# Kernel tuning notes

Hardware: AMD Instinct MI355X
Metric: run time of the kernel (lower is better)

## Reference

```python
import jax, jax.numpy as jnp
import numpy as np

TOP_K = 2
CAPACITY_FACTOR = 1.25
LOAD_BALANCE_WEIGHT = 0.01
ROUTER_Z_WEIGHT = 0.001


def setup_inputs() -> dict:
    key = jax.random.key(0)
    k1, k2, k3, k4, k5 = jax.random.split(key, 5)
    B, S, D, F, E = 4, 2048, 1024, 4096, 8
    x = jax.random.normal(k1, (B, S, D), dtype=jnp.float32)
    gate_w = jax.random.normal(k2, (E, D), dtype=jnp.float32) * 0.02
    wi_gate = jax.random.normal(k3, (E, F, D), dtype=jnp.float32) * 0.02
    wi_up = jax.random.normal(k4, (E, F, D), dtype=jnp.float32) * 0.02
    wo = jax.random.normal(k5, (E, D, F), dtype=jnp.float32) * 0.02
    return {"x": x, "gate_w": gate_w, "wi_gate": wi_gate, "wi_up": wi_up, "wo": wo}


def _dispatch_combine_one_k(x_flat, eids, ew, wi_gate, wi_up, wo, capacity):
    """Capacity-limited dispatch (first-come positions), GeGLU expert, combine."""
    N, D = x_flat.shape
    E = wi_gate.shape[0]
    # position of each token within its expert's queue (count of earlier tokens
    # assigned to the same expert) -- matches the atomic counter semantics in order.
    oh = jax.nn.one_hot(eids, E, dtype=jnp.int32)            # [N, E]
    pos = jnp.cumsum(oh, axis=0) - oh                        # counts strictly before
    pos = jnp.take_along_axis(pos, eids[:, None], axis=1)[:, 0]  # [N]
    valid = pos < capacity
    pos_safe = jnp.where(valid, pos, capacity)               # overflow bucket
    # dispatched_x[e, c, :] = x of the token at slot (e, c); zeros where empty
    disp = jnp.zeros((E, capacity + 1, D), x_flat.dtype).at[eids, pos_safe].set(x_flat)
    disp = disp[:, :capacity]                                # drop overflow bucket
    # grouped GeGLU expert: batched GEMMs over experts
    gate_h = jax.nn.silu(jnp.einsum('ecd,efd->ecf', disp, wi_gate))
    up_h = jnp.einsum('ecd,efd->ecf', disp, wi_up)
    eout = jnp.einsum('ecf,edf->ecd', gate_h * up_h, wo)     # [E, cap, D]
    # combine: gather each token's expert output, weight, zero dropped tokens
    y = eout[eids, jnp.minimum(pos, capacity - 1)]           # [N, D]
    return y * (ew * valid.astype(x_flat.dtype))[:, None]


def reference(x, gate_w, wi_gate, wi_up, wo):
    B, S, D = x.shape
    E = gate_w.shape[0]
    N = B * S
    capacity = max(int(N / E * CAPACITY_FACTOR), 1)
    x_flat = x.reshape(N, D)
    router_logits = x_flat @ gate_w.T                        # [N, E]
    router_probs = jax.nn.softmax(router_logits, axis=-1)
    topk_probs, topk_idx = jax.lax.top_k(router_probs, TOP_K)
    topk_probs = topk_probs / jnp.sum(topk_probs, axis=-1, keepdims=True)
    out = jnp.zeros_like(x_flat)
    for k in range(TOP_K):
        out = out + _dispatch_combine_one_k(
            x_flat, topk_idx[:, k], topk_probs[:, k], wi_gate, wi_up, wo, capacity)
    # aux losses: Switch-style load balance + router z-loss
    density = jnp.mean(jax.nn.one_hot(topk_idx, E, dtype=x.dtype).sum(axis=1), axis=0) / TOP_K
    mean_probs = jnp.mean(router_probs, axis=0)
    lb_loss = LOAD_BALANCE_WEIGHT * E * jnp.sum(density * mean_probs)
    z_loss = ROUTER_Z_WEIGHT * jnp.mean(jax.scipy.special.logsumexp(router_logits, axis=-1) ** 2)
    aux_loss = lb_loss + z_loss
    return out.reshape(B, S, D), aux_loss
```

## Files before the change

kernel.cpp:

```cpp
#include <hip/hip_runtime.h>
#include <cstdint>
#include <cstddef>

#define N_TOK 8192
#define DDIM  1024
#define FDIM  4096
#define NEXP  8
#define CAP   1280
#define MPE   2560
#define NSLOT (NEXP * MPE)

typedef __attribute__((ext_vector_type(8))) __bf16 bf16x8;
typedef __attribute__((ext_vector_type(4))) float  f32x4;

__device__ __forceinline__ unsigned short f2bf(float f) {
    unsigned int u = __float_as_uint(f);
    u += 0x7fffu + ((u >> 16) & 1u);
    return (unsigned short)(u >> 16);
}
__device__ __forceinline__ float bf2f(unsigned short s) {
    return __uint_as_float(((unsigned int)s) << 16);
}

__device__ __forceinline__ void async_cp16(const void* g, void* l) {
    __builtin_amdgcn_global_load_lds(
        (const __attribute__((address_space(1))) unsigned int*)g,
        (__attribute__((address_space(3))) unsigned int*)l, 16, 0, 0);
}

__global__ __launch_bounds__(256) void convert_wi_kernel(
    const float* __restrict__ wi_gate, const float* __restrict__ wi_up,
    unsigned short* __restrict__ wcomb)
{
    const int idx = blockIdx.x * 256 + threadIdx.x;
    const int d8 = idx & 127;
    const int r  = (idx >> 7) & 8191;
    const int e  = idx >> 20;
    const int f  = (r >> 7) * 64 + (r & 63);
    const float* src = (((r >> 6) & 1) ? wi_up : wi_gate)
                       + ((size_t)(e * FDIM + f) * DDIM + d8 * 8);
    const float4 a = ((const float4*)src)[0];
    const float4 b = ((const float4*)src)[1];
    uint4 o;
    o.x = (unsigned)f2bf(a.x) | ((unsigned)f2bf(a.y) << 16);
    o.y = (unsigned)f2bf(a.z) | ((unsigned)f2bf(a.w) << 16);
    o.z = (unsigned)f2bf(b.x) | ((unsigned)f2bf(b.y) << 16);
    o.w = (unsigned)f2bf(b.z) | ((unsigned)f2bf(b.w) << 16);
    *(uint4*)(wcomb + (size_t)idx * 8) = o;
}

__global__ __launch_bounds__(256) void convert_wo_kernel(
    const float* __restrict__ wo, unsigned short* __restrict__ wo_bf)
{
    const int idx = blockIdx.x * 256 + threadIdx.x;
    const float4 a = ((const float4*)(wo + (size_t)idx * 8))[0];
    const float4 b = ((const float4*)(wo + (size_t)idx * 8))[1];
    uint4 o;
    o.x = (unsigned)f2bf(a.x) | ((unsigned)f2bf(a.y) << 16);
    o.y = (unsigned)f2bf(a.z) | ((unsigned)f2bf(a.w) << 16);
    o.z = (unsigned)f2bf(b.x) | ((unsigned)f2bf(b.y) << 16);
    o.w = (unsigned)f2bf(b.z) | ((unsigned)f2bf(b.w) << 16);
    *(uint4*)(wo_bf + (size_t)idx * 8) = o;
}

__global__ __launch_bounds__(256) void router_kernel(
    const float* __restrict__ x, const float* __restrict__ gate_w,
    int* __restrict__ topk_idx, float* __restrict__ topk_w,
    float* __restrict__ stats)
{
    const int wave = threadIdx.x >> 6, lane = threadIdx.x & 63;
    const int n = blockIdx.x * 4 + wave;
    const float4* xp = (const float4*)(x + (size_t)n * DDIM + lane * 16);
    float4 xv[4];
#pragma unroll
    for (int i = 0; i < 4; i++) xv[i] = xp[i];
    float part[NEXP];
#pragma unroll
    for (int e = 0; e < NEXP; e++) {
        const float4* gp = (const float4*)(gate_w + (size_t)e * DDIM + lane * 16);
        float s = 0.f;
#pragma unroll
        for (int i = 0; i < 4; i++) {
            const float4 g = gp[i];
            s += xv[i].x * g.x + xv[i].y * g.y + xv[i].z * g.z + xv[i].w * g.w;
        }
        part[e] = s;
    }
#pragma unroll
    for (int off = 32; off > 0; off >>= 1)
#pragma unroll
        for (int e = 0; e < NEXP; e++) part[e] += __shfl_down(part[e], off);
    if (lane == 0) {
        float p[NEXP];
        float m = -1e30f;
#pragma unroll
        for (int e = 0; e < NEXP; e++) m = fmaxf(m, part[e]);
        float sum = 0.f;
#pragma unroll
        for (int e = 0; e < NEXP; e++) { p[e] = __expf(part[e] - m); sum += p[e]; }
        const float inv = 1.f / sum;
#pragma unroll
        for (int e = 0; e < NEXP; e++) p[e] *= inv;
        const float lse = m + __logf(sum);
        int e1 = 0; float p1 = p[0];
#pragma unroll
        for (int e = 1; e < NEXP; e++) if (p[e] > p1) { p1 = p[e]; e1 = e; }
        int e2 = -1; float p2 = -1.f;
#pragma unroll
        for (int e = 0; e < NEXP; e++) if (e != e1 && p[e] > p2) { p2 = p[e]; e2 = e; }
        const float wsum = p1 + p2;
        topk_idx[n * 2 + 0] = e1; topk_idx[n * 2 + 1] = e2;
        topk_w[n * 2 + 0] = p1 / wsum; topk_w[n * 2 + 1] = p2 / wsum;
        float* sp = stats + (n & 63) * 17;
#pragma unroll
        for (int e = 0; e < NEXP; e++) atomicAdd(sp + e, p[e]);
        atomicAdd(sp + 8 + e1, 1.f);
        atomicAdd(sp + 8 + e2, 1.f);
        atomicAdd(sp + 16, lse * lse);
    }
}

__global__ __launch_bounds__(512) void pos_kernel(
    const int* __restrict__ topk_idx, const float* __restrict__ topk_w,
    int* __restrict__ slot_tok, int* __restrict__ tok2slot, int* __restrict__ gcnt)
{
    __shared__ int cnt[2][NEXP][256];
    const int t = threadIdx.x;
    for (int i = t; i < NSLOT; i += 512) slot_tok[i] = -1;
    const int kk = t >> 8;
    const int c  = t & 255;
    int lc[NEXP];
#pragma unroll
    for (int e = 0; e < NEXP; e++) lc[e] = 0;
    const int base_n = c * 32;
    for (int i = 0; i < 32; i++) lc[topk_idx[(base_n + i) * 2 + kk]]++;
#pragma unroll
    for (int e = 0; e < NEXP; e++) cnt[kk][e][c] = lc[e];
    __syncthreads();
    if (t < 16) {
        const int k2 = t >> 3, e = t & 7;
        int run = 0;
        for (int c2 = 0; c2 < 256; c2++) { int v = cnt[k2][e][c2]; cnt[k2][e][c2] = run; run += v; }
        gcnt[e * 2 + k2] = run < CAP ? run : CAP;
    }
    __syncthreads();
    int run[NEXP];
#pragma unroll
    for (int e = 0; e < NEXP; e++) run[e] = cnt[kk][e][c];
    for (int i = 0; i < 32; i++) {
        const int n = base_n + i;
        const int e = topk_idx[n * 2 + kk];
        const int p = run[e]++;
        if (p < CAP) {
            const int slot = (e * 2 + kk) * CAP + p;
            slot_tok[slot] = n;
            tok2slot[n * 2 + kk] = slot;
        } else {
            tok2slot[n * 2 + kk] = -1;
        }
    }
}

__global__ __launch_bounds__(128) void dispatch_kernel(
    const float* __restrict__ x, const int* __restrict__ slot_tok,
    unsigned short* __restrict__ disp)
{
    const int slot = blockIdx.x;
    const int t = threadIdx.x;
    const int token = slot_tok[slot];
    uint4 o = make_uint4(0u, 0u, 0u, 0u);
    if (token >= 0) {
        const float4* src = (const float4*)(x + (size_t)token * DDIM + t * 8);
        const float4 a = src[0];
        const float4 b = src[1];
        o.x = (unsigned)f2bf(a.x) | ((unsigned)f2bf(a.y) << 16);
        o.y = (unsigned)f2bf(a.z) | ((unsigned)f2bf(a.w) << 16);
        o.z = (unsigned)f2bf(b.x) | ((unsigned)f2bf(b.y) << 16);
        o.w = (unsigned)f2bf(b.z) | ((unsigned)f2bf(b.w) << 16);
    }
    *(uint4*)(disp + (size_t)slot * DDIM + t * 8) = o;
}

__global__ __launch_bounds__(256, 3) void gemm1_kernel(
    const unsigned short* __restrict__ disp,
    const unsigned short* __restrict__ wcomb,
    const int* __restrict__ gcnt,
    unsigned short* __restrict__ act)
{
    __shared__ __align__(16) unsigned short smem[8704];
    const int b = blockIdx.x;
    const int e   = b / 1280;
    const int rem = b % 1280;
    const int mb = rem / 64, nb = rem % 64;
    const int kk = mb / 10;
    if ((mb % 10) * 128 >= gcnt[e * 2 + kk]) return;

    const int t = threadIdx.x;
    const int wave = t >> 6, lane = t & 63;
    const unsigned short* Asrc = disp  + (size_t)(e * MPE + mb * 128) * DDIM;
    const unsigned short* Bsrc = wcomb + (size_t)e * 8192 * DDIM + (size_t)(nb * 128) * DDIM;

    const int arow = t >> 2;
    const int acol = (((t & 3) ^ ((arow >> 1) & 3)) * 8);

    const f32x4 fzero = {0.f, 0.f, 0.f, 0.f};
    f32x4 acc[4][4];
#pragma unroll
    for (int i = 0; i < 4; i++)
#pragma unroll
        for (int j = 0; j < 4; j++) acc[i][j] = fzero;

    const int wm = wave >> 1, wn = wave & 1;
    const int lrow = lane & 15, lk = lane >> 4;
    const int lkx = (lk ^ ((lrow >> 1) & 3)) * 8;

    for (int k0 = 0; k0 < DDIM; k0 += 32) {
        __syncthreads();
        async_cp16(Asrc + (size_t)arow * DDIM + k0 + acol,        &smem[wave * 512]);
        async_cp16(Asrc + (size_t)(arow + 64) * DDIM + k0 + acol, &smem[2048 + wave * 512]);
        async_cp16(Bsrc + (size_t)arow * DDIM + k0 + acol,        &smem[4096 + wave * 512]);
        async_cp16(Bsrc + (size_t)(arow + 64) * DDIM + k0 + acol, &smem[6144 + wave * 512]);
        __syncthreads();
        bf16x8 af[4], bfr[4];
#pragma unroll
        for (int i = 0; i < 4; i++)
            af[i] = *(const bf16x8*)&smem[(wm * 64 + i * 16 + lrow) * 32 + lkx];
#pragma unroll
        for (int j = 0; j < 4; j++)
            bfr[j] = *(const bf16x8*)&smem[4096 + (wn * 64 + j * 16 + lrow) * 32 + lkx];
#pragma unroll
        for (int i = 0; i < 4; i++)
#pragma unroll
            for (int j = 0; j < 4; j++)
                acc[i][j] = __builtin_amdgcn_mfma_f32_16x16x32_bf16(af[i], bfr[j], acc[i][j], 0, 0, 0);
    }

    __syncthreads();
    if (wn == 0) {
#pragma unroll
        for (int i = 0; i < 4; i++)
#pragma unroll
            for (int j = 0; j < 4; j++)
#pragma unroll
                for (int r = 0; r < 4; r++)
                    smem[(wm * 64 + i * 16 + lk * 4 + r) * 68 + j * 16 + lrow] = f2bf(acc[i][j][r]);
    }
    __syncthreads();
    if (wn == 1) {
#pragma unroll
        for (int i = 0; i < 4; i++)
#pragma unroll
            for (int r = 0; r < 4; r++) {
                const int m = wm * 64 + i * 16 + lk * 4 + r;
                const size_t base = (size_t)(e * MPE + mb * 128 + m) * FDIM + nb * 64;
#pragma unroll
                for (int j = 0; j < 4; j++) {
                    const float g = bf2f(smem[m * 68 + j * 16 + lrow]);
                    const float u = acc[i][j][r];
                    const float a = (g / (1.f + __expf(-g))) * u;
                    act[base + j * 16 + lrow] = f2bf(a);
                }
            }
    }
}

__global__ __launch_bounds__(256, 3) void gemm2_kernel(
    const unsigned short* __restrict__ act,
    const unsigned short* __restrict__ wo_bf,
    const int* __restrict__ gcnt,
    unsigned short* __restrict__ eout)
{
    __shared__ __align__(16) unsigned short smem[8192];
    const int b = blockIdx.x;
    const int e   = b / 160;
    const int rem = b % 160;
    const int mb = rem / 8, nb = rem % 8;
    const int kk = mb / 10;
    if ((mb % 10) * 128 >= gcnt[e * 2 + kk]) return;

    const int t = threadIdx.x;
    const int wave = t >> 6, lane = t & 63;
    const unsigned short* Asrc = act   + (size_t)(e * MPE + mb * 128) * FDIM;
    const unsigned short* Bsrc = wo_bf + (size_t)e * DDIM * FDIM + (size_t)(nb * 128) * FDIM;

    const int arow = t >> 2;
    const int acol = (((t & 3) ^ ((arow >> 1) & 3)) * 8);

    const f32x4 fzero = {0.f, 0.f, 0.f, 0.f};
    f32x4 acc[4][4];
#pragma unroll
    for (int i = 0; i < 4; i++)
#pragma unroll
        for (int j = 0; j < 4; j++) acc[i][j] = fzero;

    const int wm = wave >> 1, wn = wave & 1;
    const int lrow = lane & 15, lk = lane >> 4;
    const int lkx = (lk ^ ((lrow >> 1) & 3)) * 8;

    for (int k0 = 0; k0 < FDIM; k0 += 32) {
        __syncthreads();
        async_cp16(Asrc + (size_t)arow * FDIM + k0 + acol,        &smem[wave * 512]);
        async_cp16(Asrc + (size_t)(arow + 64) * FDIM + k0 + acol, &smem[2048 + wave * 512]);
        async_cp16(Bsrc + (size_t)arow * FDIM + k0 + acol,        &smem[4096 + wave * 512]);
        async_cp16(Bsrc + (size_t)(arow + 64) * FDIM + k0 + acol, &smem[6144 + wave * 512]);
        __syncthreads();
        bf16x8 af[4], bfr[4];
#pragma unroll
        for (int i = 0; i < 4; i++)
            af[i] = *(const bf16x8*)&smem[(wm * 64 + i * 16 + lrow) * 32 + lkx];
#pragma unroll
        for (int j = 0; j < 4; j++)
            bfr[j] = *(const bf16x8*)&smem[4096 + (wn * 64 + j * 16 + lrow) * 32 + lkx];
#pragma unroll
        for (int i = 0; i < 4; i++)
#pragma unroll
            for (int j = 0; j < 4; j++)
                acc[i][j] = __builtin_amdgcn_mfma_f32_16x16x32_bf16(af[i], bfr[j], acc[i][j], 0, 0, 0);
    }
#pragma unroll
    for (int i = 0; i < 4; i++)
#pragma unroll
        for (int r = 0; r < 4; r++) {
            const int srow = e * MPE + mb * 128 + wm * 64 + i * 16 + lk * 4 + r;
            const size_t obase = (size_t)srow * DDIM + nb * 128 + wn * 64;
#pragma unroll
            for (int j = 0; j < 4; j++)
                eout[obase + j * 16 + lrow] = f2bf(acc[i][j][r]);
        }
}

__global__ __launch_bounds__(256) void combine_kernel(
    const unsigned short* __restrict__ eout,
    const int* __restrict__ tok2slot, const float* __restrict__ topk_w,
    float* __restrict__ out)
{
    const int n = blockIdx.x;
    const int t = threadIdx.x;
    const int s0 = tok2slot[n * 2 + 0], s1 = tok2slot[n * 2 + 1];
    const float w0 = (s0 >= 0) ? topk_w[n * 2 + 0] : 0.f;
    const float w1 = (s1 >= 0) ? topk_w[n * 2 + 1] : 0.f;
    const int a0 = (s0 >= 0) ? s0 : 0;
    const int a1 = (s1 >= 0) ? s1 : 0;
    const uint2 p0 = *(const uint2*)(eout + (size_t)a0 * DDIM + t * 4);
    const uint2 p1 = *(const uint2*)(eout + (size_t)a1 * DDIM + t * 4);
    float4 o;
    o.x = w0 * bf2f((unsigned short)(p0.x & 0xffff)) + w1 * bf2f((unsigned short)(p1.x & 0xffff));
    o.y = w0 * bf2f((unsigned short)(p0.x >> 16))    + w1 * bf2f((unsigned short)(p1.x >> 16));
    o.z = w0 * bf2f((unsigned short)(p0.y & 0xffff)) + w1 * bf2f((unsigned short)(p1.y & 0xffff));
    o.w = w0 * bf2f((unsigned short)(p0.y >> 16))    + w1 * bf2f((unsigned short)(p1.y >> 16));
    *(float4*)(out + (size_t)n * DDIM + t * 4) = o;
}

__global__ void aux_kernel(const float* __restrict__ stats, float* __restrict__ out)
{
    if (threadIdx.x == 0 && blockIdx.x == 0) {
        float ps[NEXP], cn[NEXP], z = 0.f;
#pragma unroll
        for (int e = 0; e < NEXP; e++) { ps[e] = 0.f; cn[e] = 0.f; }
        for (int c = 0; c < 64; c++) {
            const float* sp = stats + c * 17;
#pragma unroll
            for (int e = 0; e < NEXP; e++) { ps[e] += sp[e]; cn[e] += sp[8 + e]; }
            z += sp[16];
        }
        float lb = 0.f;
#pragma unroll
        for (int e = 0; e < NEXP; e++)
            lb += (cn[e] / (2.f * N_TOK)) * (ps[e] / N_TOK);
        const float aux = 0.01f * 8.f * lb + 0.001f * (z / N_TOK);
        out[(size_t)N_TOK * DDIM] = aux;
    }
}

extern "C" void kernel_launch(void* const* d_in, const int* in_sizes, int n_in,
                              void* d_out, int out_size, void* d_ws, size_t ws_size,
                              hipStream_t stream)
{
    (void)in_sizes; (void)n_in; (void)ws_size; (void)out_size;
    const float* x       = (const float*)d_in[0];
    const float* gate_w  = (const float*)d_in[1];
    const float* wi_gate = (const float*)d_in[2];
    const float* wi_up   = (const float*)d_in[3];
    const float* wo      = (const float*)d_in[4];
    float* out = (float*)d_out;
    char* ws = (char*)d_ws;

    int*            topk_idx = (int*)(ws + 0);
    float*          topk_w   = (float*)(ws + 65536);
    int*            slot_tok = (int*)(ws + 131072);
    int*            tok2slot = (int*)(ws + 212992);
    float*          stats    = (float*)(ws + 278528);
    int*            gcnt     = (int*)(ws + 282880);
    unsigned short* disp     = (unsigned short*)(ws + 524288);
    unsigned short* act      = (unsigned short*)(ws + 42467328);
    unsigned short* eout     = (unsigned short*)(ws + 210239488);
    unsigned short* wcomb    = (unsigned short*)(ws + 252182528);
    unsigned short* wo_bf    = (unsigned short*)(ws + 386400256);

    hipMemsetAsync(stats, 0, 64 * 17 * sizeof(float), stream);

    convert_wi_kernel<<<32768, 256, 0, stream>>>(wi_gate, wi_up, wcomb);
    convert_wo_kernel<<<16384, 256, 0, stream>>>(wo, wo_bf);
    router_kernel<<<N_TOK / 4, 256, 0, stream>>>(x, gate_w, topk_idx, topk_w, stats);
    pos_kernel<<<1, 512, 0, stream>>>(topk_idx, topk_w, slot_tok, tok2slot, gcnt);
    dispatch_kernel<<<NSLOT, 128, 0, stream>>>(x, slot_tok, disp);
    gemm1_kernel<<<NEXP * 20 * 64, 256, 0, stream>>>(disp, wcomb, gcnt, act);
    gemm2_kernel<<<NEXP * 20 * 8, 256, 0, stream>>>(act, wo_bf, gcnt, eout);
    combine_kernel<<<N_TOK, 256, 0, stream>>>(eout, tok2slot, topk_w, out);
    aux_kernel<<<1, 64, 0, stream>>>(stats, out);
}
```

Measured before the change: 1.116 ms.

## Enlarge gemm1 tiles to 256x256 with triple-buffered async LDS pipeline

Rewrites the first expert GEMM so each 512-thread block computes a 256x256 tile instead of 128x128. K-tiles are staged into LDS through a three-deep ring of async copies, with split A/B prefetches interleaved between MFMA halves and s_setprio raised around the compute. The aim is to raise arithmetic intensity and hide global load latency behind MFMA work. In exchange, LDS and register use grow (96KB LDS, 128 accumulator floats per thread), which cuts occupancy, and capacity skipping becomes coarser at 256-row granularity.

```diff
diff --git a/kernel.cpp b/kernel.cpp
--- a/kernel.cpp
+++ b/kernel.cpp
@@ -181,83 +181,124 @@
     *(uint4*)(disp + (size_t)slot * DDIM + t * 8) = o;
 }
 
-__global__ __launch_bounds__(256, 3) void gemm1_kernel(
+__global__ __launch_bounds__(512, 2) void gemm1_kernel(
     const unsigned short* __restrict__ disp,
     const unsigned short* __restrict__ wcomb,
     const int* __restrict__ gcnt,
     unsigned short* __restrict__ act)
 {
-    __shared__ __align__(16) unsigned short smem[8704];
+    __shared__ __align__(16) unsigned short smem[49152];
     const int b = blockIdx.x;
-    const int e   = b / 1280;
-    const int rem = b % 1280;
-    const int mb = rem / 64, nb = rem % 64;
-    const int kk = mb / 10;
-    if ((mb % 10) * 128 >= gcnt[e * 2 + kk]) return;
+    const int e    = b / 320;
+    const int rem  = b % 320;
+    const int kk   = rem / 160;
+    const int rem2 = rem % 160;
+    const int mt = rem2 / 32, nt = rem2 % 32;
+    if (mt * 256 >= gcnt[e * 2 + kk]) return;
 
     const int t = threadIdx.x;
     const int wave = t >> 6, lane = t & 63;
-    const unsigned short* Asrc = disp  + (size_t)(e * MPE + mb * 128) * DDIM;
-    const unsigned short* Bsrc = wcomb + (size_t)e * 8192 * DDIM + (size_t)(nb * 128) * DDIM;
-
-    const int arow = t >> 2;
-    const int acol = (((t & 3) ^ ((arow >> 1) & 3)) * 8);
-
-    const f32x4 fzero = {0.f, 0.f, 0.f, 0.f};
-    f32x4 acc[4][4];
-#pragma unroll
-    for (int i = 0; i < 4; i++)
-#pragma unroll
-        for (int j = 0; j < 4; j++) acc[i][j] = fzero;
-
-    const int wm = wave >> 1, wn = wave & 1;
+    const unsigned short* Asrc = disp  + (size_t)(e * MPE + kk * CAP + mt * 256) * DDIM;
+    const unsigned short* Bsrc = wcomb + (size_t)e * 8192 * DDIM + (size_t)(nt * 256) * DDIM;
+
+    const int srow = t >> 2;
+    const int qg   = (((t & 3) ^ ((srow >> 1) & 3)) * 8);
+    const size_t soff0 = (size_t)srow * DDIM + qg;
+    const size_t soff1 = (size_t)(srow + 128) * DDIM + qg;
+    const int lb0 = wave * 512;
+    const int lb1 = 4096 + wave * 512;
+
+#define G1_STAGE_A(c, kt) do { \
+        async_cp16(Asrc + soff0 + (size_t)(kt) * 32, &smem[(c) * 16384 + lb0]); \
+        async_cp16(Asrc + soff1 + (size_t)(kt) * 32, &smem[(c) * 16384 + lb1]); } while (0)
+#define G1_STAGE_B(c, kt) do { \
+        async_cp16(Bsrc + soff0 + (size_t)(kt) * 32, &smem[(c) * 16384 + 8192 + lb0]); \
+        async_cp16(Bsrc + soff1 + (size_t)(kt) * 32, &smem[(c) * 16384 + 8192 + lb1]); } while (0)
+
+    const int wm = wave >> 2, wn = wave & 3;
     const int lrow = lane & 15, lk = lane >> 4;
     const int lkx = (lk ^ ((lrow >> 1) & 3)) * 8;
-
-    for (int k0 = 0; k0 < DDIM; k0 += 32) {
-        __syncthreads();
-        async_cp16(Asrc + (size_t)arow * DDIM + k0 + acol,        &smem[wave * 512]);
-        async_cp16(Asrc + (size_t)(arow + 64) * DDIM + k0 + acol, &smem[2048 + wave * 512]);
-        async_cp16(Bsrc + (size_t)arow * DDIM + k0 + acol,        &smem[4096 + wave * 512]);
-        async_cp16(Bsrc + (size_t)(arow + 64) * DDIM + k0 + acol, &smem[6144 + wave * 512]);
-        __syncthreads();
+    const int aro = (wm * 128 + lrow) * 32 + lkx;
+    const int bro = 8192 + (wn * 64 + lrow) * 32 + lkx;
+
+    const f32x4 fzero = {0.f, 0.f, 0.f, 0.f};
+    f32x4 acc[8][4];
+#pragma unroll
+    for (int i = 0; i < 8; i++)
+#pragma unroll
+        for (int j = 0; j < 4; j++) acc[i][j] = fzero;
+
+    G1_STAGE_A(0, 0); G1_STAGE_B(0, 0);
+    G1_STAGE_A(1, 1); G1_STAGE_B(1, 1);
+    asm volatile("s_waitcnt vmcnt(4)" ::: "memory");
+    __builtin_amdgcn_s_barrier();
+
+    int cur = 0;
+#pragma unroll 1
+    for (int kt = 0; kt < 32; ++kt) {
+        const int cbase = cur * 16384;
+        int cnxt = cur + 2; if (cnxt >= 3) cnxt -= 3;
+        const bool pf = (kt + 2 < 32);
         bf16x8 af[4], bfr[4];
 #pragma unroll
-        for (int i = 0; i < 4; i++)
-            af[i] = *(const bf16x8*)&smem[(wm * 64 + i * 16 + lrow) * 32 + lkx];
-#pragma unroll
-        for (int j = 0; j < 4; j++)
-            bfr[j] = *(const bf16x8*)&smem[4096 + (wn * 64 + j * 16 + lrow) * 32 + lkx];
+        for (int i = 0; i < 4; i++) af[i]  = *(const bf16x8*)&smem[cbase + aro + i * 512];
+#pragma unroll
+        for (int j = 0; j < 4; j++) bfr[j] = *(const bf16x8*)&smem[cbase + bro + j * 512];
+        if (pf) G1_STAGE_A(cnxt, kt + 2);
+        __builtin_amdgcn_s_barrier();
+        __builtin_amdgcn_s_setprio(1);
 #pragma unroll
         for (int i = 0; i < 4; i++)
 #pragma unroll
             for (int j = 0; j < 4; j++)
                 acc[i][j] = __builtin_amdgcn_mfma_f32_16x16x32_bf16(af[i], bfr[j], acc[i][j], 0, 0, 0);
-    }
+        __builtin_amdgcn_s_setprio(0);
+        __builtin_amdgcn_s_barrier();
+        bf16x8 ag[4];
+#pragma unroll
+        for (int i = 0; i < 4; i++) ag[i] = *(const bf16x8*)&smem[cbase + aro + (i + 4) * 512];
+        if (pf) G1_STAGE_B(cnxt, kt + 2);
+        __builtin_amdgcn_s_barrier();
+        __builtin_amdgcn_s_setprio(1);
+#pragma unroll
+        for (int i = 0; i < 4; i++)
+#pragma unroll
+            for (int j = 0; j < 4; j++)
+                acc[i + 4][j] = __builtin_amdgcn_mfma_f32_16x16x32_bf16(ag[i], bfr[j], acc[i + 4][j], 0, 0, 0);
+        __builtin_amdgcn_s_setprio(0);
+        if (pf) asm volatile("s_waitcnt vmcnt(4)" ::: "memory");
+        else    asm volatile("s_waitcnt vmcnt(0)" ::: "memory");
+        __builtin_amdgcn_s_barrier();
+        cur = cur + 1; if (cur == 3) cur = 0;
+    }
+#undef G1_STAGE_A
+#undef G1_STAGE_B
 
     __syncthreads();
-    if (wn == 0) {
-#pragma unroll
-        for (int i = 0; i < 4; i++)
+    const int g = wn >> 1;
+    const int epb = g * 17408;
+    if ((wn & 1) == 0) {
+#pragma unroll
+        for (int i = 0; i < 8; i++)
 #pragma unroll
             for (int j = 0; j < 4; j++)
 #pragma unroll
                 for (int r = 0; r < 4; r++)
-                    smem[(wm * 64 + i * 16 + lk * 4 + r) * 68 + j * 16 + lrow] = f2bf(acc[i][j][r]);
+                    smem[epb + (wm * 128 + i * 16 + lk * 4 + r) * 68 + j * 16 + lrow] = f2bf(acc[i][j][r]);
     }
     __syncthreads();
-    if (wn == 1) {
-#pragma unroll
-        for (int i = 0; i < 4; i++)
+    if (wn & 1) {
+#pragma unroll
+        for (int i = 0; i < 8; i++)
 #pragma unroll
             for (int r = 0; r < 4; r++) {
-                const int m = wm * 64 + i * 16 + lk * 4 + r;
-                const size_t base = (size_t)(e * MPE + mb * 128 + m) * FDIM + nb * 64;
+                const int m = wm * 128 + i * 16 + lk * 4 + r;
+                const size_t base = (size_t)(e * MPE + kk * CAP + mt * 256 + m) * FDIM + (nt * 2 + g) * 64;
 #pragma unroll
                 for (int j = 0; j < 4; j++) {
-                    const float g = bf2f(smem[m * 68 + j * 16 + lrow]);
-                    const float u = acc[i][j][r];
-                    const float a = (g / (1.f + __expf(-g))) * u;
+                    const float gv = bf2f(smem[epb + m * 68 + j * 16 + lrow]);
+                    const float u  = acc[i][j][r];
+                    const float a  = (gv / (1.f + __expf(-gv))) * u;
                     act[base + j * 16 + lrow] = f2bf(a);
                 }
             }
@@ -404,7 +445,7 @@
     router_kernel<<<N_TOK / 4, 256, 0, stream>>>(x, gate_w, topk_idx, topk_w, stats);
     pos_kernel<<<1, 512, 0, stream>>>(topk_idx, topk_w, slot_tok, tok2slot, gcnt);
     dispatch_kernel<<<NSLOT, 128, 0, stream>>>(x, slot_tok, disp);
-    gemm1_kernel<<<NEXP * 20 * 64, 256, 0, stream>>>(disp, wcomb, gcnt, act);
+    gemm1_kernel<<<NEXP * 2 * 5 * 32, 512, 0, stream>>>(disp, wcomb, gcnt, act);
     gemm2_kernel<<<NEXP * 20 * 8, 256, 0, stream>>>(act, wo_bf, gcnt, eout);
     combine_kernel<<<N_TOK, 256, 0, stream>>>(eout, tok2slot, topk_w, out);
     aux_kernel<<<1, 64, 0, stream>>>(stats, out);
```

New measurement: 1.147 ms. +2.8%, slower.

## Replace expert GEMMs with 256x256-tile, 4-stage pipelined 512-thread template kernel

Applied to the files above, without the earlier changes.

Both expert GEMMs (gate/up with GeGLU epilogue, and down projection) are replaced by one templated kernel. It uses 256x256 output tiles, 8 waves per block and a 4-deep LDS ring of async copies with explicit vmcnt waits, plus register double-buffered fragment reads. This is meant to raise data reuse per tile and overlap global loads with MFMA, instead of the old synchronous single-stage 128x128 loop. In exchange it uses 128KB of shared memory per block, which limits occupancy. The larger tiles also mean fewer blocks, coarser capacity skipping and more padded rows.

```diff
diff --git a/kernel.cpp b/kernel.cpp
--- a/kernel.cpp
+++ b/kernel.cpp
@@ -181,152 +181,135 @@
     *(uint4*)(disp + (size_t)slot * DDIM + t * 8) = o;
 }
 
-__global__ __launch_bounds__(256, 3) void gemm1_kernel(
-    const unsigned short* __restrict__ disp,
-    const unsigned short* __restrict__ wcomb,
+template<int KDIM, int BROWS, int NT, int EPI>
+__global__ __launch_bounds__(512, 2) void gemm256(
+    const unsigned short* __restrict__ A,
+    const unsigned short* __restrict__ Bw,
     const int* __restrict__ gcnt,
-    unsigned short* __restrict__ act)
-{
-    __shared__ __align__(16) unsigned short smem[8704];
+    unsigned short* __restrict__ outp)
+{
+    constexpr int NKT = KDIM / 32;
+    __shared__ __align__(16) unsigned short smem[65536];
     const int b = blockIdx.x;
-    const int e   = b / 1280;
-    const int rem = b % 1280;
-    const int mb = rem / 64, nb = rem % 64;
-    const int kk = mb / 10;
-    if ((mb % 10) * 128 >= gcnt[e * 2 + kk]) return;
+    const int e    = b / (2 * 5 * NT);
+    const int rem  = b % (2 * 5 * NT);
+    const int kk   = rem / (5 * NT);
+    const int rem2 = rem % (5 * NT);
+    const int mt = rem2 / NT, nt = rem2 % NT;
+    if (mt * 256 >= gcnt[e * 2 + kk]) return;
 
     const int t = threadIdx.x;
     const int wave = t >> 6, lane = t & 63;
-    const unsigned short* Asrc = disp  + (size_t)(e * MPE + mb * 128) * DDIM;
-    const unsigned short* Bsrc = wcomb + (size_t)e * 8192 * DDIM + (size_t)(nb * 128) * DDIM;
-
-    const int arow = t >> 2;
-    const int acol = (((t & 3) ^ ((arow >> 1) & 3)) * 8);
-
-    const f32x4 fzero = {0.f, 0.f, 0.f, 0.f};
-    f32x4 acc[4][4];
-#pragma unroll
-    for (int i = 0; i < 4; i++)
-#pragma unroll
-        for (int j = 0; j < 4; j++) acc[i][j] = fzero;
-
-    const int wm = wave >> 1, wn = wave & 1;
+    const unsigned short* Asrc = A  + (size_t)(e * MPE + kk * CAP + mt * 256) * KDIM;
+    const unsigned short* Bsrc = Bw + ((size_t)e * BROWS + (size_t)nt * 256) * KDIM;
+
+    const int srow = t >> 2;
+    const int qg   = (((t & 3) ^ ((srow >> 1) & 3)) * 8);
+    const size_t soff0 = (size_t)srow * KDIM + qg;
+    const size_t soff1 = (size_t)(srow + 128) * KDIM + qg;
+    const int lb0 = wave * 512, lb1 = 4096 + wave * 512;
+
+#define STG(c, kt) do { \
+        const size_t ko_ = (size_t)(kt) * 32; \
+        async_cp16(Asrc + soff0 + ko_, &smem[(c) * 16384 + lb0]); \
+        async_cp16(Asrc + soff1 + ko_, &smem[(c) * 16384 + lb1]); \
+        async_cp16(Bsrc + soff0 + ko_, &smem[(c) * 16384 + 8192 + lb0]); \
+        async_cp16(Bsrc + soff1 + ko_, &smem[(c) * 16384 + 8192 + lb1]); } while (0)
+
+    const int wm = wave >> 2, wn = wave & 3;
     const int lrow = lane & 15, lk = lane >> 4;
     const int lkx = (lk ^ ((lrow >> 1) & 3)) * 8;
-
-    for (int k0 = 0; k0 < DDIM; k0 += 32) {
+    const int aro = (wm * 128 + lrow) * 32 + lkx;
+    const int bro = 8192 + (wn * 64 + lrow) * 32 + lkx;
+
+    const f32x4 fzero = {0.f, 0.f, 0.f, 0.f};
+    f32x4 acc[8][4];
+#pragma unroll
+    for (int i = 0; i < 8; i++)
+#pragma unroll
+        for (int j = 0; j < 4; j++) acc[i][j] = fzero;
+
+#define RD(SA, SB, c) do { \
+        _Pragma("unroll") for (int i_ = 0; i_ < 8; i_++) \
+            SA[i_] = *(const bf16x8*)&smem[(c) * 16384 + aro + i_ * 512]; \
+        _Pragma("unroll") for (int j_ = 0; j_ < 4; j_++) \
+            SB[j_] = *(const bf16x8*)&smem[(c) * 16384 + bro + j_ * 512]; } while (0)
+
+#define MM(SA, SB) do { \
+        __builtin_amdgcn_s_setprio(1); \
+        _Pragma("unroll") for (int i_ = 0; i_ < 8; i_++) \
+            _Pragma("unroll") for (int j_ = 0; j_ < 4; j_++) \
+                acc[i_][j_] = __builtin_amdgcn_mfma_f32_16x16x32_bf16(SA[i_], SB[j_], acc[i_][j_], 0, 0, 0); \
+        __builtin_amdgcn_s_setprio(0); } while (0)
+
+#define BODY(kt, CA, CB, NA, NB) do { \
+        if ((kt) < NKT - 2) asm volatile("s_waitcnt vmcnt(4)" ::: "memory"); \
+        else                asm volatile("s_waitcnt vmcnt(0)" ::: "memory"); \
+        __builtin_amdgcn_s_barrier(); \
+        if ((kt) + 1 < NKT) RD(NA, NB, ((kt) + 1) & 3); \
+        if ((kt) + 3 < NKT) STG(((kt) + 3) & 3, (kt) + 3); \
+        __builtin_amdgcn_sched_barrier(0); \
+        MM(CA, CB); } while (0)
+
+    STG(0, 0); STG(1, 1); STG(2, 2);
+    asm volatile("s_waitcnt vmcnt(8)" ::: "memory");
+    __builtin_amdgcn_s_barrier();
+
+    bf16x8 afA[8], bfA[4], afB[8], bfB[4];
+    RD(afA, bfA, 0);
+
+#pragma unroll 1
+    for (int m = 0; m < NKT / 2; m++) {
+        BODY(2 * m,     afA, bfA, afB, bfB);
+        BODY(2 * m + 1, afB, bfB, afA, bfA);
+    }
+#undef BODY
+#undef MM
+#undef RD
+#undef STG
+
+    if constexpr (EPI == 1) {
         __syncthreads();
-        async_cp16(Asrc + (size_t)arow * DDIM + k0 + acol,        &smem[wave * 512]);
-        async_cp16(Asrc + (size_t)(arow + 64) * DDIM + k0 + acol, &smem[2048 + wave * 512]);
-        async_cp16(Bsrc + (size_t)arow * DDIM + k0 + acol,        &smem[4096 + wave * 512]);
-        async_cp16(Bsrc + (size_t)(arow + 64) * DDIM + k0 + acol, &smem[6144 + wave * 512]);
+        const int g = wn >> 1;
+        const int epb = g * 17408;
+        if ((wn & 1) == 0) {
+#pragma unroll
+            for (int i = 0; i < 8; i++)
+#pragma unroll
+                for (int j = 0; j < 4; j++)
+#pragma unroll
+                    for (int r = 0; r < 4; r++)
+                        smem[epb + (wm * 128 + i * 16 + lk * 4 + r) * 68 + j * 16 + lrow] = f2bf(acc[i][j][r]);
+        }
         __syncthreads();
-        bf16x8 af[4], bfr[4];
-#pragma unroll
-        for (int i = 0; i < 4; i++)
-            af[i] = *(const bf16x8*)&smem[(wm * 64 + i * 16 + lrow) * 32 + lkx];
-#pragma unroll
-        for (int j = 0; j < 4; j++)
-            bfr[j] = *(const bf16x8*)&smem[4096 + (wn * 64 + j * 16 + lrow) * 32 + lkx];
-#pragma unroll
-        for (int i = 0; i < 4; i++)
-#pragma unroll
-            for (int j = 0; j < 4; j++)
-                acc[i][j] = __builtin_amdgcn_mfma_f32_16x16x32_bf16(af[i], bfr[j], acc[i][j], 0, 0, 0);
-    }
-
-    __syncthreads();
-    if (wn == 0) {
-#pragma unroll
-        for (int i = 0; i < 4; i++)
-#pragma unroll
-            for (int j = 0; j < 4; j++)
-#pragma unroll
-                for (int r = 0; r < 4; r++)
-                    smem[(wm * 64 + i * 16 + lk * 4 + r) * 68 + j * 16 + lrow] = f2bf(acc[i][j][r]);
-    }
-    __syncthreads();
-    if (wn == 1) {
-#pragma unroll
-        for (int i = 0; i < 4; i++)
+        if (wn & 1) {
+#pragma unroll
+            for (int i = 0; i < 8; i++)
+#pragma unroll
+                for (int r = 0; r < 4; r++) {
+                    const int mrow = wm * 128 + i * 16 + lk * 4 + r;
+                    const size_t base = (size_t)(e * MPE + kk * CAP + mt * 256 + mrow) * FDIM + (nt * 2 + g) * 64;
+#pragma unroll
+                    for (int j = 0; j < 4; j++) {
+                        const float gv = bf2f(smem[epb + mrow * 68 + j * 16 + lrow]);
+                        const float u  = acc[i][j][r];
+                        const float a  = (gv / (1.f + __expf(-gv))) * u;
+                        outp[base + j * 16 + lrow] = f2bf(a);
+                    }
+                }
+        }
+    } else {
+#pragma unroll
+        for (int i = 0; i < 8; i++)
 #pragma unroll
             for (int r = 0; r < 4; r++) {
-                const int m = wm * 64 + i * 16 + lk * 4 + r;
-                const size_t base = (size_t)(e * MPE + mb * 128 + m) * FDIM + nb * 64;
-#pragma unroll
-                for (int j = 0; j < 4; j++) {
-                    const float g = bf2f(smem[m * 68 + j * 16 + lrow]);
-                    const float u = acc[i][j][r];
-                    const float a = (g / (1.f + __expf(-g))) * u;
-                    act[base + j * 16 + lrow] = f2bf(a);
-                }
+                const int orow = e * MPE + kk * CAP + mt * 256 + wm * 128 + i * 16 + lk * 4 + r;
+                const size_t obase = (size_t)orow * DDIM + nt * 256 + wn * 64;
+#pragma unroll
+                for (int j = 0; j < 4; j++)
+                    outp[obase + j * 16 + lrow] = f2bf(acc[i][j][r]);
             }
     }
-}
-
-__global__ __launch_bounds__(256, 3) void gemm2_kernel(
-    const unsigned short* __restrict__ act,
-    const unsigned short* __restrict__ wo_bf,
-    const int* __restrict__ gcnt,
-    unsigned short* __restrict__ eout)
-{
-    __shared__ __align__(16) unsigned short smem[8192];
-    const int b = blockIdx.x;
-    const int e   = b / 160;
-    const int rem = b % 160;
-    const int mb = rem / 8, nb = rem % 8;
-    const int kk = mb / 10;
-    if ((mb % 10) * 128 >= gcnt[e * 2 + kk]) return;
-
-    const int t = threadIdx.x;
-    const int wave = t >> 6, lane = t & 63;
-    const unsigned short* Asrc = act   + (size_t)(e * MPE + mb * 128) * FDIM;
-    const unsigned short* Bsrc = wo_bf + (size_t)e * DDIM * FDIM + (size_t)(nb * 128) * FDIM;
-
-    const int arow = t >> 2;
-    const int acol = (((t & 3) ^ ((arow >> 1) & 3)) * 8);
-
-    const f32x4 fzero = {0.f, 0.f, 0.f, 0.f};
-    f32x4 acc[4][4];
-#pragma unroll
-    for (int i = 0; i < 4; i++)
-#pragma unroll
-        for (int j = 0; j < 4; j++) acc[i][j] = fzero;
-
-    const int wm = wave >> 1, wn = wave & 1;
-    const int lrow = lane & 15, lk = lane >> 4;
-    const int lkx = (lk ^ ((lrow >> 1) & 3)) * 8;
-
-    for (int k0 = 0; k0 < FDIM; k0 += 32) {
-        __syncthreads();
-        async_cp16(Asrc + (size_t)arow * FDIM + k0 + acol,        &smem[wave * 512]);
-        async_cp16(Asrc + (size_t)(arow + 64) * FDIM + k0 + acol, &smem[2048 + wave * 512]);
-        async_cp16(Bsrc + (size_t)arow * FDIM + k0 + acol,        &smem[4096 + wave * 512]);
-        async_cp16(Bsrc + (size_t)(arow + 64) * FDIM + k0 + acol, &smem[6144 + wave * 512]);
-        __syncthreads();
-        bf16x8 af[4], bfr[4];
-#pragma unroll
-        for (int i = 0; i < 4; i++)
-            af[i] = *(const bf16x8*)&smem[(wm * 64 + i * 16 + lrow) * 32 + lkx];
-#pragma unroll
-        for (int j = 0; j < 4; j++)
-            bfr[j] = *(const bf16x8*)&smem[4096 + (wn * 64 + j * 16 + lrow) * 32 + lkx];
-#pragma unroll
-        for (int i = 0; i < 4; i++)
-#pragma unroll
-            for (int j = 0; j < 4; j++)
-                acc[i][j] = __builtin_amdgcn_mfma_f32_16x16x32_bf16(af[i], bfr[j], acc[i][j], 0, 0, 0);
-    }
-#pragma unroll
-    for (int i = 0; i < 4; i++)
-#pragma unroll
-        for (int r = 0; r < 4; r++) {
-            const int srow = e * MPE + mb * 128 + wm * 64 + i * 16 + lk * 4 + r;
-            const size_t obase = (size_t)srow * DDIM + nb * 128 + wn * 64;
-#pragma unroll
-            for (int j = 0; j < 4; j++)
-                eout[obase + j * 16 + lrow] = f2bf(acc[i][j][r]);
-        }
 }
 
 __global__ __launch_bounds__(256) void combine_kernel(
@@ -404,8 +387,8 @@
     router_kernel<<<N_TOK / 4, 256, 0, stream>>>(x, gate_w, topk_idx, topk_w, stats);
     pos_kernel<<<1, 512, 0, stream>>>(topk_idx, topk_w, slot_tok, tok2slot, gcnt);
     dispatch_kernel<<<NSLOT, 128, 0, stream>>>(x, slot_tok, disp);
-    gemm1_kernel<<<NEXP * 20 * 64, 256, 0, stream>>>(disp, wcomb, gcnt, act);
-    gemm2_kernel<<<NEXP * 20 * 8, 256, 0, stream>>>(act, wo_bf, gcnt, eout);
+    gemm256<1024, 8192, 32, 1><<<NEXP * 2 * 5 * 32, 512, 0, stream>>>(disp, wcomb, gcnt, act);
+    gemm256<4096, 1024, 4, 0><<<NEXP * 2 * 5 * 4, 512, 0, stream>>>(act, wo_bf, gcnt, eout);
     combine_kernel<<<N_TOK, 256, 0, stream>>>(eout, tok2slot, topk_w, out);
     aux_kernel<<<1, 64, 0, stream>>>(stats, out);
 }
```

Result: no change. 1.101 ms (-1.4%).
